# Performance work log

Measured on AMD Instinct MI355X. Metric: run time of the kernel, lower is better.

## Reference

```python
import jax, jax.numpy as jnp
import numpy as np

B, S, D, H, DFF, L = 16, 1024, 64, 4, 256, 2
DEPTH = D // H
C1, C2, NOUT = 64, 64, 1
EPS = 1e-6


def setup_inputs() -> dict:
    key = jax.random.key(0)
    ks = jax.random.split(key, 24)
    s = 0.02
    vals = jax.random.normal(ks[0], (B, S), jnp.float32)
    nanp = jax.random.uniform(ks[1], (B, S)) < 0.1
    inputs = jnp.where(nanp, jnp.nan, vals)
    inp = {
        'inputs': inputs,
        'embedding': jax.random.normal(ks[2], (S, D - 1), jnp.float32) * s,
        'wq': jax.random.normal(ks[3], (L, D, D), jnp.float32) * s,
        'wq_b': jnp.zeros((L, D), jnp.float32),
        'wk': jax.random.normal(ks[4], (L, D, D), jnp.float32) * s,
        'wk_b': jnp.zeros((L, D), jnp.float32),
        'wv': jax.random.normal(ks[5], (L, D, D), jnp.float32) * s,
        'wv_b': jnp.zeros((L, D), jnp.float32),
        'wo': jax.random.normal(ks[6], (L, D, D), jnp.float32) * s,
        'ffn_w1': jax.random.normal(ks[7], (L, D, DFF), jnp.float32) * s,
        'ffn_w2': jax.random.normal(ks[8], (L, DFF, D), jnp.float32) * s,
        'ln1_g': jnp.ones((L, D), jnp.float32),
        'ln1_b': jnp.zeros((L, D), jnp.float32),
        'ln2_g': jnp.ones((L, D), jnp.float32),
        'ln2_b': jnp.zeros((L, D), jnp.float32),
        'c_w1': jax.random.normal(ks[9], (D, C1), jnp.float32) * s,
        'c_b1': jnp.zeros((C1,), jnp.float32),
        'c_w2': jax.random.normal(ks[10], (C1, C2), jnp.float32) * s,
        'c_b2': jnp.zeros((C2,), jnp.float32),
        'c_w3': jax.random.normal(ks[11], (C2, NOUT), jnp.float32) * s,
        'c_b3': jnp.zeros((NOUT,), jnp.float32),
        'out_bias': jax.random.normal(ks[12], (1, NOUT), jnp.float32),
    }
    return inp


def _layer_norm(x, g, b):
    m = jnp.mean(x, axis=-1, keepdims=True)
    v = jnp.mean((x - m) ** 2, axis=-1, keepdims=True)
    return (x - m) / jnp.sqrt(v + EPS) * g + b


def _forward(inputs, embedding, wq, wq_b, wk, wk_b, wv, wv_b, wo,
             ffn_w1, ffn_w2, ln1_g, ln1_b, ln2_g, ln2_b,
             c_w1, c_b1, c_w2, c_b2, c_w3, c_b3, out_bias):
    nan_mask = jnp.isnan(inputs)                           # (B,S) bool
    x_in = jnp.where(nan_mask, jnp.zeros_like(inputs), inputs)
    # mask (B,1,S,S): masked if either attribute i or j is NaN
    mask = (nan_mask[:, :, None] | nan_mask[:, None, :]).astype(jnp.float32)[:, None, :, :]
    # keep factor: zeros out NaN attribute rows after each sub-block  (B,S,1)
    keep = 1.0 - jnp.transpose(jnp.prod(mask, axis=-1), (0, 2, 1))

    # positional/attribute embedding: table * sqrt(d-1) * sqrt(d)
    attr = embedding * jnp.sqrt(jnp.float32(D - 1)) * jnp.sqrt(jnp.float32(D))  # (S, D-1)
    attr = jnp.broadcast_to(attr[None], (B, S, D - 1))
    x = jnp.concatenate([attr, x_in[:, :, None]], axis=2)  # (B,S,D)
    x = x * keep

    scale = 1.0 / jnp.sqrt(jnp.float32(DEPTH))
    for i in range(L):
        q = (x @ wq[i] + wq_b[i]).reshape(B, S, H, DEPTH).transpose(0, 2, 1, 3)
        k = (x @ wk[i] + wk_b[i]).reshape(B, S, H, DEPTH).transpose(0, 2, 1, 3)
        v = (x @ wv[i] + wv_b[i]).reshape(B, S, H, DEPTH).transpose(0, 2, 1, 3)
        logits = jnp.einsum('bhqd,bhkd->bhqk', q, k) * scale + mask * (-1e9)
        attn = jax.nn.softmax(logits, axis=-1) * (1.0 - mask)  # post-softmax multiplicative mask
        ctx = jnp.einsum('bhqk,bhkd->bhqd', attn, v)
        ctx = ctx.transpose(0, 2, 1, 3).reshape(B, S, D) @ wo[i]
        out1 = _layer_norm(x + ctx, ln1_g[i], ln1_b[i]) * keep
        ffn = jax.nn.relu(out1 @ ffn_w1[i]) @ ffn_w2[i]
        x = _layer_norm(out1 + ffn, ln2_g[i], ln2_b[i]) * keep

    h = jax.nn.relu(x @ c_w1 + c_b1)
    h = jax.nn.relu(h @ c_w2 + c_b2)
    phi = h @ c_w3 + c_b3                                   # (B,S,NOUT)
    y = jnp.sum(phi, axis=1) + out_bias                     # (B,NOUT)
    return y


def reference(inputs, embedding, wq, wq_b, wk, wk_b, wv, wv_b, wo,
              ffn_w1, ffn_w2, ln1_g, ln1_b, ln2_g, ln2_b,
              c_w1, c_b1, c_w2, c_b2, c_w3, c_b3, out_bias):
    return _forward(inputs, embedding, wq, wq_b, wk, wk_b, wv, wv_b, wo,
                    ffn_w1, ffn_w2, ln1_g, ln1_b, ln2_g, ln2_b,
                    c_w1, c_b1, c_w2, c_b2, c_w3, c_b3, out_bias)
```

## Files before the change

### kernel.cpp

```cpp
#include <hip/hip_runtime.h>
#include <hip/hip_bf16.h>
#include <math.h>

#define BB 16
#define SS 1024
#define DD 64
#define HH 4
#define DEPTH 16
#define DFF 256
#define NROWS (BB*SS)
#define EPSV 1e-6f
#define NKSPLIT 8
#define KCHUNK (SS / NKSPLIT)

__device__ __forceinline__ float bcast(float x, int kk) {
  return __int_as_float(__builtin_amdgcn_readlane(__float_as_int(x), kk));
}

__global__ __launch_bounds__(256) void build_x_kernel(
    const float* __restrict__ inputs, const float* __restrict__ emb,
    float* __restrict__ x, float* __restrict__ keep) {
  int gid = blockIdx.x * 256 + threadIdx.x;
  int row = gid >> 6;
  int d = gid & 63;
  int s = row & (SS - 1);
  float vin = inputs[row];
  bool nan = __builtin_isnan(vin);
  float kp = nan ? 0.0f : 1.0f;
  if (d == 0) keep[row] = kp;
  float val;
  if (d < 63) {
    const float scale = 7.93725393319377f * 8.0f;
    val = emb[s * 63 + d] * scale;
  } else {
    val = nan ? 0.0f : vin;
  }
  x[row * 64 + d] = val * kp;
}

__global__ __launch_bounds__(64, 2) void qkv_kernel(
    const float* __restrict__ xin,
    const float* __restrict__ wq, const float* __restrict__ wqb,
    const float* __restrict__ wk, const float* __restrict__ wkb,
    const float* __restrict__ wv, const float* __restrict__ wvb,
    float* __restrict__ q, float* __restrict__ k, float* __restrict__ v) {
  int lane = threadIdx.x;
  float wqc[64], wkc[64], wvc[64];
#pragma unroll
  for (int kk = 0; kk < 64; ++kk) {
    wqc[kk] = wq[kk * 64 + lane];
    wkc[kk] = wk[kk * 64 + lane];
    wvc[kk] = wv[kk * 64 + lane];
  }
  float bq = wqb[lane], bk = wkb[lane], bv = wvb[lane];
  int h = lane >> 4, dep = lane & 15;
  int row0 = blockIdx.x * 8;
  for (int r = row0; r < row0 + 8; ++r) {
    float xr = xin[r * 64 + lane];
    float qa0 = 0.f, qa1 = 0.f, ka0 = 0.f, ka1 = 0.f, va0 = 0.f, va1 = 0.f;
#pragma unroll
    for (int kk = 0; kk < 64; kk += 2) {
      float x0 = bcast(xr, kk);
      float x1 = bcast(xr, kk + 1);
      qa0 = fmaf(x0, wqc[kk], qa0); qa1 = fmaf(x1, wqc[kk + 1], qa1);
      ka0 = fmaf(x0, wkc[kk], ka0); ka1 = fmaf(x1, wkc[kk + 1], ka1);
      va0 = fmaf(x0, wvc[kk], va0); va1 = fmaf(x1, wvc[kk + 1], va1);
    }
    int b = r >> 10, s = r & (SS - 1);
    size_t o = (size_t)(((b * HH + h) * SS + s)) * DEPTH + dep;
    q[o] = qa0 + qa1 + bq;
    k[o] = ka0 + ka1 + bk;
    v[o] = va0 + va1 + bv;
  }
}

__global__ __launch_bounds__(256) void attn_partial_kernel(
    const float* __restrict__ q, const float* __restrict__ k,
    const float* __restrict__ v, const float* __restrict__ keep,
    float* __restrict__ pA, float* __restrict__ pL) {
  __shared__ float klds[KCHUNK * DEPTH];
  __shared__ float vlds[KCHUNK * DEPTH];
  __shared__ float kplds[KCHUNK];
  int tid = threadIdx.x;
  int p = blockIdx.x * 256 + tid;
  int c = blockIdx.y;
  int bh = p >> 9;
  int s0 = p & 511;
  int b = bh >> 2;

  const float4* kbase = (const float4*)(k + ((size_t)bh * SS + c * KCHUNK) * DEPTH);
  const float4* vbase = (const float4*)(v + ((size_t)bh * SS + c * KCHUNK) * DEPTH);
#pragma unroll
  for (int i = 0; i < KCHUNK * 4 / 256; ++i) {
    ((float4*)klds)[tid + i * 256] = kbase[tid + i * 256];
    ((float4*)vlds)[tid + i * 256] = vbase[tid + i * 256];
  }
  if (tid < KCHUNK) kplds[tid] = keep[b * SS + c * KCHUNK + tid];
  __syncthreads();

  size_t rowA = (size_t)bh * SS + s0;
  size_t rowB = rowA + 512;
  const float4* qa4 = (const float4*)(q + rowA * DEPTH);
  const float4* qb4 = (const float4*)(q + rowB * DEPTH);
  float4 qA0 = qa4[0], qA1 = qa4[1], qA2 = qa4[2], qA3 = qa4[3];
  float4 qB0 = qb4[0], qB1 = qb4[1], qB2 = qb4[2], qB3 = qb4[3];
  float4 z = make_float4(0.f, 0.f, 0.f, 0.f);
  float4 aA0 = z, aA1 = z, aA2 = z, aA3 = z;
  float4 aB0 = z, aB1 = z, aB2 = z, aB3 = z;
  float lA = 0.0f, lB = 0.0f;
  for (int j = 0; j < KCHUNK; ++j) {
    const float4* kl = (const float4*)&klds[j * DEPTH];
    float4 k0 = kl[0], k1 = kl[1], k2 = kl[2], k3 = kl[3];
    const float4* vl = (const float4*)&vlds[j * DEPTH];
    float4 v0 = vl[0], v1 = vl[1], v2 = vl[2], v3 = vl[3];
    float dA0 = qA0.x * k0.x, dA1 = qA2.x * k2.x;
    float dB0 = qB0.x * k0.x, dB1 = qB2.x * k2.x;
    dA0 = fmaf(qA0.y, k0.y, dA0); dA1 = fmaf(qA2.y, k2.y, dA1);
    dB0 = fmaf(qB0.y, k0.y, dB0); dB1 = fmaf(qB2.y, k2.y, dB1);
    dA0 = fmaf(qA0.z, k0.z, dA0); dA1 = fmaf(qA2.z, k2.z, dA1);
    dB0 = fmaf(qB0.z, k0.z, dB0); dB1 = fmaf(qB2.z, k2.z, dB1);
    dA0 = fmaf(qA0.w, k0.w, dA0); dA1 = fmaf(qA2.w, k2.w, dA1);
    dB0 = fmaf(qB0.w, k0.w, dB0); dB1 = fmaf(qB2.w, k2.w, dB1);
    dA0 = fmaf(qA1.x, k1.x, dA0); dA1 = fmaf(qA3.x, k3.x, dA1);
    dB0 = fmaf(qB1.x, k1.x, dB0); dB1 = fmaf(qB3.x, k3.x, dB1);
    dA0 = fmaf(qA1.y, k1.y, dA0); dA1 = fmaf(qA3.y, k3.y, dA1);
    dB0 = fmaf(qB1.y, k1.y, dB0); dB1 = fmaf(qB3.y, k3.y, dB1);
    dA0 = fmaf(qA1.z, k1.z, dA0); dA1 = fmaf(qA3.z, k3.z, dA1);
    dB0 = fmaf(qB1.z, k1.z, dB0); dB1 = fmaf(qB3.z, k3.z, dB1);
    dA0 = fmaf(qA1.w, k1.w, dA0); dA1 = fmaf(qA3.w, k3.w, dA1);
    dB0 = fmaf(qB1.w, k1.w, dB0); dB1 = fmaf(qB3.w, k3.w, dB1);
    float kpj = kplds[j];
    float pa = __expf((dA0 + dA1) * 0.25f) * kpj;
    float pb = __expf((dB0 + dB1) * 0.25f) * kpj;
    lA += pa; lB += pb;
    aA0.x = fmaf(pa, v0.x, aA0.x); aB0.x = fmaf(pb, v0.x, aB0.x);
    aA0.y = fmaf(pa, v0.y, aA0.y); aB0.y = fmaf(pb, v0.y, aB0.y);
    aA0.z = fmaf(pa, v0.z, aA0.z); aB0.z = fmaf(pb, v0.z, aB0.z);
    aA0.w = fmaf(pa, v0.w, aA0.w); aB0.w = fmaf(pb, v0.w, aB0.w);
    aA1.x = fmaf(pa, v1.x, aA1.x); aB1.x = fmaf(pb, v1.x, aB1.x);
    aA1.y = fmaf(pa, v1.y, aA1.y); aB1.y = fmaf(pb, v1.y, aB1.y);
    aA1.z = fmaf(pa, v1.z, aA1.z); aB1.z = fmaf(pb, v1.z, aB1.z);
    aA1.w = fmaf(pa, v1.w, aA1.w); aB1.w = fmaf(pb, v1.w, aB1.w);
    aA2.x = fmaf(pa, v2.x, aA2.x); aB2.x = fmaf(pb, v2.x, aB2.x);
    aA2.y = fmaf(pa, v2.y, aA2.y); aB2.y = fmaf(pb, v2.y, aB2.y);
    aA2.z = fmaf(pa, v2.z, aA2.z); aB2.z = fmaf(pb, v2.z, aB2.z);
    aA2.w = fmaf(pa, v2.w, aA2.w); aB2.w = fmaf(pb, v2.w, aB2.w);
    aA3.x = fmaf(pa, v3.x, aA3.x); aB3.x = fmaf(pb, v3.x, aB3.x);
    aA3.y = fmaf(pa, v3.y, aA3.y); aB3.y = fmaf(pb, v3.y, aB3.y);
    aA3.z = fmaf(pa, v3.z, aA3.z); aB3.z = fmaf(pb, v3.z, aB3.z);
    aA3.w = fmaf(pa, v3.w, aA3.w); aB3.w = fmaf(pb, v3.w, aB3.w);
  }
  size_t oA = ((size_t)c << 16) + rowA;
  size_t oB = ((size_t)c << 16) + rowB;
  pL[oA] = lA; pL[oB] = lB;
  float4* o4a = (float4*)(pA + oA * 16);
  o4a[0] = aA0; o4a[1] = aA1; o4a[2] = aA2; o4a[3] = aA3;
  float4* o4b = (float4*)(pA + oB * 16);
  o4b[0] = aB0; o4b[1] = aB1; o4b[2] = aB2; o4b[3] = aB3;
}

__global__ __launch_bounds__(256) void wo_ln1_kernel(
    const float* __restrict__ pA, const float* __restrict__ pL,
    const float* __restrict__ xin,
    const float* __restrict__ wo, const float* __restrict__ g,
    const float* __restrict__ bta, const float* __restrict__ keep,
    float* __restrict__ out1) {
  int tid = threadIdx.x;
  int lane = tid & 63;
  float woc[64];
#pragma unroll
  for (int kk = 0; kk < 64; ++kk) woc[kk] = wo[kk * 64 + lane];
  float gg = g[lane], bb = bta[lane];
  int wave = tid >> 6;
  int row0 = blockIdx.x * 16 + wave * 4;
  for (int r = row0; r < row0 + 4; ++r) {
    int b = r >> 10, s = r & (SS - 1);
    int h = lane >> 4, dep = lane & 15;
    size_t rowi = ((size_t)(b * HH + h) << 10) + s;
    float num = 0.0f, den = 0.0f;
#pragma unroll
    for (int c = 0; c < NKSPLIT; ++c) {
      num += pA[(((size_t)c << 16) + rowi) * 16 + dep];
      den += pL[((size_t)c << 16) + rowi];
    }
    float cr = num * keep[r] / den;
    float a0 = 0.f, a1 = 0.f;
#pragma unroll
    for (int kk = 0; kk < 64; kk += 2) {
      a0 = fmaf(bcast(cr, kk), woc[kk], a0);
      a1 = fmaf(bcast(cr, kk + 1), woc[kk + 1], a1);
    }
    float t = a0 + a1 + xin[r * 64 + lane];
    float sum = t;
#pragma unroll
    for (int off = 32; off; off >>= 1) sum += __shfl_xor(sum, off, 64);
    float mean = sum * (1.0f / 64.0f);
    float dv = t - mean;
    float sq = dv * dv;
#pragma unroll
    for (int off = 32; off; off >>= 1) sq += __shfl_xor(sq, off, 64);
    float var = sq * (1.0f / 64.0f);
    float o = dv * rsqrtf(var + EPSV) * gg + bb;
    out1[r * 64 + lane] = o * keep[r];
  }
}

__global__ __launch_bounds__(256) void ffn_fused_kernel(
    const float* __restrict__ out1, const float* __restrict__ w1,
    const float* __restrict__ w2, const float* __restrict__ g,
    const float* __restrict__ bta, const float* __restrict__ keep,
    float* __restrict__ xout) {
  __shared__ float part[4][4][64];
  int tid = threadIdx.x, wave = tid >> 6, lane = tid & 63;
  float w1c[64], w2c[64];
#pragma unroll
  for (int kk = 0; kk < 64; ++kk)
    w1c[kk] = w1[kk * 256 + wave * 64 + lane];
#pragma unroll
  for (int j = 0; j < 64; ++j)
    w2c[j] = w2[(wave * 64 + j) * 64 + lane];
  float gg = g[lane], bb = bta[lane];
  int row0 = blockIdx.x * 16;
  for (int grp = 0; grp < 4; ++grp) {
    int rbase = row0 + grp * 4;
    float xr0 = out1[(rbase + 0) * 64 + lane];
    float xr1 = out1[(rbase + 1) * 64 + lane];
    float xr2 = out1[(rbase + 2) * 64 + lane];
    float xr3 = out1[(rbase + 3) * 64 + lane];
    float xrs[4] = {xr0, xr1, xr2, xr3};
#pragma unroll
    for (int r = 0; r < 4; ++r) {
      float h0 = 0.f, h1 = 0.f;
#pragma unroll
      for (int kk = 0; kk < 64; kk += 2) {
        h0 = fmaf(bcast(xrs[r], kk), w1c[kk], h0);
        h1 = fmaf(bcast(xrs[r], kk + 1), w1c[kk + 1], h1);
      }
      float hv = fmaxf(h0 + h1, 0.0f);
      float y0 = 0.f, y1 = 0.f;
#pragma unroll
      for (int j = 0; j < 64; j += 2) {
        y0 = fmaf(bcast(hv, j), w2c[j], y0);
        y1 = fmaf(bcast(hv, j + 1), w2c[j + 1], y1);
      }
      part[r][wave][lane] = y0 + y1;
    }
    __syncthreads();
    float xres = (wave == 0) ? xr0 : (wave == 1) ? xr1 : (wave == 2) ? xr2 : xr3;
    float t = part[wave][0][lane] + part[wave][1][lane] +
              part[wave][2][lane] + part[wave][3][lane] + xres;
    float sum = t;
#pragma unroll
    for (int off = 32; off; off >>= 1) sum += __shfl_xor(sum, off, 64);
    float mean = sum * (1.0f / 64.0f);
    float dv = t - mean;
    float sq = dv * dv;
#pragma unroll
    for (int off = 32; off; off >>= 1) sq += __shfl_xor(sq, off, 64);
    float var = sq * (1.0f / 64.0f);
    float o = dv * rsqrtf(var + EPSV) * gg + bb;
    xout[(rbase + wave) * 64 + lane] = o * keep[rbase + wave];
    __syncthreads();
  }
}

__global__ void init_out_kernel(const float* __restrict__ out_bias,
                                float* __restrict__ out) {
  if (threadIdx.x < BB) out[threadIdx.x] = out_bias[0];
}

__global__ __launch_bounds__(256, 3) void classifier_kernel(
    const float* __restrict__ x,
    const float* __restrict__ w1, const float* __restrict__ b1,
    const float* __restrict__ w2, const float* __restrict__ b2,
    const float* __restrict__ w3, const float* __restrict__ b3,
    float* __restrict__ out) {
  int tid = threadIdx.x;
  int lane = tid & 63, wave = tid >> 6;
  float w1c[64], w2c[64];
#pragma unroll
  for (int kk = 0; kk < 64; ++kk) {
    w1c[kk] = w1[kk * 64 + lane];
    w2c[kk] = w2[kk * 64 + lane];
  }
  float w3d = w3[lane];
  float bb1 = b1[lane], bb2 = b2[lane], b3v = b3[0];
  int row0 = blockIdx.x * 32 + wave * 8;
  float wavesum = 0.0f;
  for (int r = row0; r < row0 + 8; ++r) {
    float xr = x[r * 64 + lane];
    float h1a = 0.f, h1b = 0.f;
#pragma unroll
    for (int kk = 0; kk < 64; kk += 2) {
      h1a = fmaf(bcast(xr, kk), w1c[kk], h1a);
      h1b = fmaf(bcast(xr, kk + 1), w1c[kk + 1], h1b);
    }
    float h1 = fmaxf(h1a + h1b + bb1, 0.0f);
    float h2a = 0.f, h2b = 0.f;
#pragma unroll
    for (int kk = 0; kk < 64; kk += 2) {
      h2a = fmaf(bcast(h1, kk), w2c[kk], h2a);
      h2b = fmaf(bcast(h1, kk + 1), w2c[kk + 1], h2b);
    }
    float h2 = fmaxf(h2a + h2b + bb2, 0.0f);
    float p = h2 * w3d;
#pragma unroll
    for (int off = 32; off; off >>= 1) p += __shfl_xor(p, off, 64);
    wavesum += p + b3v;
  }
  if (lane == 0) {
    int b = row0 >> 10;
    atomicAdd(&out[b], wavesum);
  }
}

extern "C" void kernel_launch(void* const* d_in, const int* in_sizes, int n_in,
                              void* d_out, int out_size, void* d_ws, size_t ws_size,
                              hipStream_t stream) {
  const float* inputs = (const float*)d_in[0];
  const float* emb    = (const float*)d_in[1];
  const float* wq     = (const float*)d_in[2];
  const float* wqb    = (const float*)d_in[3];
  const float* wk     = (const float*)d_in[4];
  const float* wkb    = (const float*)d_in[5];
  const float* wv     = (const float*)d_in[6];
  const float* wvb    = (const float*)d_in[7];
  const float* wo     = (const float*)d_in[8];
  const float* fw1    = (const float*)d_in[9];
  const float* fw2    = (const float*)d_in[10];
  const float* l1g    = (const float*)d_in[11];
  const float* l1b    = (const float*)d_in[12];
  const float* l2g    = (const float*)d_in[13];
  const float* l2b    = (const float*)d_in[14];
  const float* cw1    = (const float*)d_in[15];
  const float* cb1    = (const float*)d_in[16];
  const float* cw2    = (const float*)d_in[17];
  const float* cb2    = (const float*)d_in[18];
  const float* cw3    = (const float*)d_in[19];
  const float* cb3    = (const float*)d_in[20];
  const float* obias  = (const float*)d_in[21];
  float* out = (float*)d_out;

  float* ws   = (float*)d_ws;
  float* x    = ws;
  float* keep = x    + (size_t)NROWS * 64;
  float* q    = keep + NROWS;
  float* k    = q    + (size_t)NROWS * 64;
  float* v    = k    + (size_t)NROWS * 64;
  float* out1 = v    + (size_t)NROWS * 64;
  float* pA   = out1 + (size_t)NROWS * 64;
  float* pL   = pA   + (size_t)NKSPLIT * 65536 * 16;

  build_x_kernel<<<4096, 256, 0, stream>>>(inputs, emb, x, keep);

  for (int i = 0; i < 2; ++i) {
    qkv_kernel<<<2048, 64, 0, stream>>>(
        x, wq + i * 4096, wqb + i * 64, wk + i * 4096, wkb + i * 64,
        wv + i * 4096, wvb + i * 64, q, k, v);
    attn_partial_kernel<<<dim3(128, NKSPLIT), 256, 0, stream>>>(
        q, k, v, keep, pA, pL);
    wo_ln1_kernel<<<1024, 256, 0, stream>>>(
        pA, pL, x, wo + i * 4096, l1g + i * 64, l1b + i * 64, keep, out1);
    ffn_fused_kernel<<<1024, 256, 0, stream>>>(
        out1, fw1 + i * 16384, fw2 + i * 16384, l2g + i * 64, l2b + i * 64,
        keep, x);
  }

  init_out_kernel<<<1, 64, 0, stream>>>(obias, out);
  classifier_kernel<<<512, 256, 0, stream>>>(x, cw1, cb1, cw2, cb2, cw3, cb3, out);
}
```

Baseline: 424.4 us.

## Use one query per attention thread and uniform float4 row loads in matvecs

The attention partial kernel now handles one query row per thread instead of two. It doubles the grid and adds a launch bound of 8 blocks per CU to raise occupancy, at the cost of reloading K/V tiles into LDS twice as often. The qkv, FFN and classifier kernels drop the readlane broadcast of a per-lane row element. They instead load the whole input row as wave-uniform float4 reads, trading cross-lane broadcasts for redundant cached memory loads.

```diff
diff --git a/kernel.cpp b/kernel.cpp
--- a/kernel.cpp
+++ b/kernel.cpp
@@ -56,15 +56,17 @@
   int h = lane >> 4, dep = lane & 15;
   int row0 = blockIdx.x * 8;
   for (int r = row0; r < row0 + 8; ++r) {
-    float xr = xin[r * 64 + lane];
+    const float4* xu = (const float4*)&xin[r * 64];
     float qa0 = 0.f, qa1 = 0.f, ka0 = 0.f, ka1 = 0.f, va0 = 0.f, va1 = 0.f;
 #pragma unroll
-    for (int kk = 0; kk < 64; kk += 2) {
-      float x0 = bcast(xr, kk);
-      float x1 = bcast(xr, kk + 1);
-      qa0 = fmaf(x0, wqc[kk], qa0); qa1 = fmaf(x1, wqc[kk + 1], qa1);
-      ka0 = fmaf(x0, wkc[kk], ka0); ka1 = fmaf(x1, wkc[kk + 1], ka1);
-      va0 = fmaf(x0, wvc[kk], va0); va1 = fmaf(x1, wvc[kk + 1], va1);
+    for (int t = 0; t < 16; ++t) {
+      float4 xv = xu[t];
+      qa0 = fmaf(xv.x, wqc[4*t+0], qa0); qa1 = fmaf(xv.y, wqc[4*t+1], qa1);
+      qa0 = fmaf(xv.z, wqc[4*t+2], qa0); qa1 = fmaf(xv.w, wqc[4*t+3], qa1);
+      ka0 = fmaf(xv.x, wkc[4*t+0], ka0); ka1 = fmaf(xv.y, wkc[4*t+1], ka1);
+      ka0 = fmaf(xv.z, wkc[4*t+2], ka0); ka1 = fmaf(xv.w, wkc[4*t+3], ka1);
+      va0 = fmaf(xv.x, wvc[4*t+0], va0); va1 = fmaf(xv.y, wvc[4*t+1], va1);
+      va0 = fmaf(xv.z, wvc[4*t+2], va0); va1 = fmaf(xv.w, wvc[4*t+3], va1);
     }
     int b = r >> 10, s = r & (SS - 1);
     size_t o = (size_t)(((b * HH + h) * SS + s)) * DEPTH + dep;
@@ -74,7 +76,7 @@
   }
 }
 
-__global__ __launch_bounds__(256) void attn_partial_kernel(
+__global__ __launch_bounds__(256, 8) void attn_partial_kernel(
     const float* __restrict__ q, const float* __restrict__ k,
     const float* __restrict__ v, const float* __restrict__ keep,
     float* __restrict__ pA, float* __restrict__ pL) {
@@ -82,10 +84,9 @@
   __shared__ float vlds[KCHUNK * DEPTH];
   __shared__ float kplds[KCHUNK];
   int tid = threadIdx.x;
-  int p = blockIdx.x * 256 + tid;
+  int grow = blockIdx.x * 256 + tid;
   int c = blockIdx.y;
-  int bh = p >> 9;
-  int s0 = p & 511;
+  int bh = grow >> 10;
   int b = bh >> 2;
 
   const float4* kbase = (const float4*)(k + ((size_t)bh * SS + c * KCHUNK) * DEPTH);
@@ -98,65 +99,39 @@
   if (tid < KCHUNK) kplds[tid] = keep[b * SS + c * KCHUNK + tid];
   __syncthreads();
 
-  size_t rowA = (size_t)bh * SS + s0;
-  size_t rowB = rowA + 512;
-  const float4* qa4 = (const float4*)(q + rowA * DEPTH);
-  const float4* qb4 = (const float4*)(q + rowB * DEPTH);
-  float4 qA0 = qa4[0], qA1 = qa4[1], qA2 = qa4[2], qA3 = qa4[3];
-  float4 qB0 = qb4[0], qB1 = qb4[1], qB2 = qb4[2], qB3 = qb4[3];
+  const float4* q4 = (const float4*)(q + (size_t)grow * DEPTH);
+  float4 q0 = q4[0], q1 = q4[1], q2 = q4[2], q3 = q4[3];
   float4 z = make_float4(0.f, 0.f, 0.f, 0.f);
-  float4 aA0 = z, aA1 = z, aA2 = z, aA3 = z;
-  float4 aB0 = z, aB1 = z, aB2 = z, aB3 = z;
-  float lA = 0.0f, lB = 0.0f;
+  float4 a0 = z, a1 = z, a2 = z, a3 = z;
+  float l = 0.0f;
   for (int j = 0; j < KCHUNK; ++j) {
     const float4* kl = (const float4*)&klds[j * DEPTH];
     float4 k0 = kl[0], k1 = kl[1], k2 = kl[2], k3 = kl[3];
     const float4* vl = (const float4*)&vlds[j * DEPTH];
     float4 v0 = vl[0], v1 = vl[1], v2 = vl[2], v3 = vl[3];
-    float dA0 = qA0.x * k0.x, dA1 = qA2.x * k2.x;
-    float dB0 = qB0.x * k0.x, dB1 = qB2.x * k2.x;
-    dA0 = fmaf(qA0.y, k0.y, dA0); dA1 = fmaf(qA2.y, k2.y, dA1);
-    dB0 = fmaf(qB0.y, k0.y, dB0); dB1 = fmaf(qB2.y, k2.y, dB1);
-    dA0 = fmaf(qA0.z, k0.z, dA0); dA1 = fmaf(qA2.z, k2.z, dA1);
-    dB0 = fmaf(qB0.z, k0.z, dB0); dB1 = fmaf(qB2.z, k2.z, dB1);
-    dA0 = fmaf(qA0.w, k0.w, dA0); dA1 = fmaf(qA2.w, k2.w, dA1);
-    dB0 = fmaf(qB0.w, k0.w, dB0); dB1 = fmaf(qB2.w, k2.w, dB1);
-    dA0 = fmaf(qA1.x, k1.x, dA0); dA1 = fmaf(qA3.x, k3.x, dA1);
-    dB0 = fmaf(qB1.x, k1.x, dB0); dB1 = fmaf(qB3.x, k3.x, dB1);
-    dA0 = fmaf(qA1.y, k1.y, dA0); dA1 = fmaf(qA3.y, k3.y, dA1);
-    dB0 = fmaf(qB1.y, k1.y, dB0); dB1 = fmaf(qB3.y, k3.y, dB1);
-    dA0 = fmaf(qA1.z, k1.z, dA0); dA1 = fmaf(qA3.z, k3.z, dA1);
-    dB0 = fmaf(qB1.z, k1.z, dB0); dB1 = fmaf(qB3.z, k3.z, dB1);
-    dA0 = fmaf(qA1.w, k1.w, dA0); dA1 = fmaf(qA3.w, k3.w, dA1);
-    dB0 = fmaf(qB1.w, k1.w, dB0); dB1 = fmaf(qB3.w, k3.w, dB1);
-    float kpj = kplds[j];
-    float pa = __expf((dA0 + dA1) * 0.25f) * kpj;
-    float pb = __expf((dB0 + dB1) * 0.25f) * kpj;
-    lA += pa; lB += pb;
-    aA0.x = fmaf(pa, v0.x, aA0.x); aB0.x = fmaf(pb, v0.x, aB0.x);
-    aA0.y = fmaf(pa, v0.y, aA0.y); aB0.y = fmaf(pb, v0.y, aB0.y);
-    aA0.z = fmaf(pa, v0.z, aA0.z); aB0.z = fmaf(pb, v0.z, aB0.z);
-    aA0.w = fmaf(pa, v0.w, aA0.w); aB0.w = fmaf(pb, v0.w, aB0.w);
-    aA1.x = fmaf(pa, v1.x, aA1.x); aB1.x = fmaf(pb, v1.x, aB1.x);
-    aA1.y = fmaf(pa, v1.y, aA1.y); aB1.y = fmaf(pb, v1.y, aB1.y);
-    aA1.z = fmaf(pa, v1.z, aA1.z); aB1.z = fmaf(pb, v1.z, aB1.z);
-    aA1.w = fmaf(pa, v1.w, aA1.w); aB1.w = fmaf(pb, v1.w, aB1.w);
-    aA2.x = fmaf(pa, v2.x, aA2.x); aB2.x = fmaf(pb, v2.x, aB2.x);
-    aA2.y = fmaf(pa, v2.y, aA2.y); aB2.y = fmaf(pb, v2.y, aB2.y);
-    aA2.z = fmaf(pa, v2.z, aA2.z); aB2.z = fmaf(pb, v2.z, aB2.z);
-    aA2.w = fmaf(pa, v2.w, aA2.w); aB2.w = fmaf(pb, v2.w, aB2.w);
-    aA3.x = fmaf(pa, v3.x, aA3.x); aB3.x = fmaf(pb, v3.x, aB3.x);
-    aA3.y = fmaf(pa, v3.y, aA3.y); aB3.y = fmaf(pb, v3.y, aB3.y);
-    aA3.z = fmaf(pa, v3.z, aA3.z); aB3.z = fmaf(pb, v3.z, aB3.z);
-    aA3.w = fmaf(pa, v3.w, aA3.w); aB3.w = fmaf(pb, v3.w, aB3.w);
-  }
-  size_t oA = ((size_t)c << 16) + rowA;
-  size_t oB = ((size_t)c << 16) + rowB;
-  pL[oA] = lA; pL[oB] = lB;
-  float4* o4a = (float4*)(pA + oA * 16);
-  o4a[0] = aA0; o4a[1] = aA1; o4a[2] = aA2; o4a[3] = aA3;
-  float4* o4b = (float4*)(pA + oB * 16);
-  o4b[0] = aB0; o4b[1] = aB1; o4b[2] = aB2; o4b[3] = aB3;
+    float d0 = q0.x * k0.x, d1 = q2.x * k2.x;
+    d0 = fmaf(q0.y, k0.y, d0); d1 = fmaf(q2.y, k2.y, d1);
+    d0 = fmaf(q0.z, k0.z, d0); d1 = fmaf(q2.z, k2.z, d1);
+    d0 = fmaf(q0.w, k0.w, d0); d1 = fmaf(q2.w, k2.w, d1);
+    d0 = fmaf(q1.x, k1.x, d0); d1 = fmaf(q3.x, k3.x, d1);
+    d0 = fmaf(q1.y, k1.y, d0); d1 = fmaf(q3.y, k3.y, d1);
+    d0 = fmaf(q1.z, k1.z, d0); d1 = fmaf(q3.z, k3.z, d1);
+    d0 = fmaf(q1.w, k1.w, d0); d1 = fmaf(q3.w, k3.w, d1);
+    float p = __expf((d0 + d1) * 0.25f) * kplds[j];
+    l += p;
+    a0.x = fmaf(p, v0.x, a0.x); a0.y = fmaf(p, v0.y, a0.y);
+    a0.z = fmaf(p, v0.z, a0.z); a0.w = fmaf(p, v0.w, a0.w);
+    a1.x = fmaf(p, v1.x, a1.x); a1.y = fmaf(p, v1.y, a1.y);
+    a1.z = fmaf(p, v1.z, a1.z); a1.w = fmaf(p, v1.w, a1.w);
+    a2.x = fmaf(p, v2.x, a2.x); a2.y = fmaf(p, v2.y, a2.y);
+    a2.z = fmaf(p, v2.z, a2.z); a2.w = fmaf(p, v2.w, a2.w);
+    a3.x = fmaf(p, v3.x, a3.x); a3.y = fmaf(p, v3.y, a3.y);
+    a3.z = fmaf(p, v3.z, a3.z); a3.w = fmaf(p, v3.w, a3.w);
+  }
+  size_t orow = ((size_t)c << 16) + grow;
+  pL[orow] = l;
+  float4* o4 = (float4*)(pA + orow * 16);
+  o4[0] = a0; o4[1] = a1; o4[2] = a2; o4[3] = a3;
 }
 
 __global__ __launch_bounds__(256) void wo_ln1_kernel(
@@ -223,18 +198,15 @@
   int row0 = blockIdx.x * 16;
   for (int grp = 0; grp < 4; ++grp) {
     int rbase = row0 + grp * 4;
-    float xr0 = out1[(rbase + 0) * 64 + lane];
-    float xr1 = out1[(rbase + 1) * 64 + lane];
-    float xr2 = out1[(rbase + 2) * 64 + lane];
-    float xr3 = out1[(rbase + 3) * 64 + lane];
-    float xrs[4] = {xr0, xr1, xr2, xr3};
 #pragma unroll
     for (int r = 0; r < 4; ++r) {
+      const float4* xu = (const float4*)&out1[(rbase + r) * 64];
       float h0 = 0.f, h1 = 0.f;
 #pragma unroll
-      for (int kk = 0; kk < 64; kk += 2) {
-        h0 = fmaf(bcast(xrs[r], kk), w1c[kk], h0);
-        h1 = fmaf(bcast(xrs[r], kk + 1), w1c[kk + 1], h1);
+      for (int t = 0; t < 16; ++t) {
+        float4 xv = xu[t];
+        h0 = fmaf(xv.x, w1c[4*t+0], h0); h1 = fmaf(xv.y, w1c[4*t+1], h1);
+        h0 = fmaf(xv.z, w1c[4*t+2], h0); h1 = fmaf(xv.w, w1c[4*t+3], h1);
       }
       float hv = fmaxf(h0 + h1, 0.0f);
       float y0 = 0.f, y1 = 0.f;
@@ -246,7 +218,7 @@
       part[r][wave][lane] = y0 + y1;
     }
     __syncthreads();
-    float xres = (wave == 0) ? xr0 : (wave == 1) ? xr1 : (wave == 2) ? xr2 : xr3;
+    float xres = out1[(rbase + wave) * 64 + lane];
     float t = part[wave][0][lane] + part[wave][1][lane] +
               part[wave][2][lane] + part[wave][3][lane] + xres;
     float sum = t;
@@ -288,12 +260,13 @@
   int row0 = blockIdx.x * 32 + wave * 8;
   float wavesum = 0.0f;
   for (int r = row0; r < row0 + 8; ++r) {
-    float xr = x[r * 64 + lane];
+    const float4* xu = (const float4*)&x[r * 64];
     float h1a = 0.f, h1b = 0.f;
 #pragma unroll
-    for (int kk = 0; kk < 64; kk += 2) {
-      h1a = fmaf(bcast(xr, kk), w1c[kk], h1a);
-      h1b = fmaf(bcast(xr, kk + 1), w1c[kk + 1], h1b);
+    for (int t = 0; t < 16; ++t) {
+      float4 xv = xu[t];
+      h1a = fmaf(xv.x, w1c[4*t+0], h1a); h1b = fmaf(xv.y, w1c[4*t+1], h1b);
+      h1a = fmaf(xv.z, w1c[4*t+2], h1a); h1b = fmaf(xv.w, w1c[4*t+3], h1b);
     }
     float h1 = fmaxf(h1a + h1b + bb1, 0.0f);
     float h2a = 0.f, h2b = 0.f;
@@ -357,7 +330,7 @@
     qkv_kernel<<<2048, 64, 0, stream>>>(
         x, wq + i * 4096, wqb + i * 64, wk + i * 4096, wkb + i * 64,
         wv + i * 4096, wvb + i * 64, q, k, v);
-    attn_partial_kernel<<<dim3(128, NKSPLIT), 256, 0, stream>>>(
+    attn_partial_kernel<<<dim3(256, NKSPLIT), 256, 0, stream>>>(
         q, k, v, keep, pA, pL);
     wo_ln1_kernel<<<1024, 256, 0, stream>>>(
         pA, pL, x, wo + i * 4096, l1g + i * 64, l1b + i * 64, keep, out1);
```

After: 627.5 us. +47.8%, slower.

## Split QKV projection across waves with LDS row staging; LDS broadcast in Wo

Applied to the files above, without the earlier changes.

The QKV kernel now gives each of three waves one of the Q/K/V weight matrices and stages 16 input rows in shared memory, so each wave holds 64 weight registers instead of 192. Row values are read as float4 from LDS instead of readlane broadcasts, and the Wo+LN1 kernel uses the same LDS broadcast for its context vector. Attention dot products are collapsed into a single accumulator chain, and occupancy hints are added to the launch bounds. The aim is less register pressure, higher occupancy and fewer scalar readlane instructions, at the cost of longer dependency chains in attention and extra LDS traffic.

```diff
diff --git a/kernel.cpp b/kernel.cpp
--- a/kernel.cpp
+++ b/kernel.cpp
@@ -38,48 +38,51 @@
   x[row * 64 + d] = val * kp;
 }
 
-__global__ __launch_bounds__(64, 2) void qkv_kernel(
+__global__ __launch_bounds__(192, 4) void qkv_kernel(
     const float* __restrict__ xin,
     const float* __restrict__ wq, const float* __restrict__ wqb,
     const float* __restrict__ wk, const float* __restrict__ wkb,
     const float* __restrict__ wv, const float* __restrict__ wvb,
     float* __restrict__ q, float* __restrict__ k, float* __restrict__ v) {
-  int lane = threadIdx.x;
-  float wqc[64], wkc[64], wvc[64];
-#pragma unroll
-  for (int kk = 0; kk < 64; ++kk) {
-    wqc[kk] = wq[kk * 64 + lane];
-    wkc[kk] = wk[kk * 64 + lane];
-    wvc[kk] = wv[kk * 64 + lane];
-  }
-  float bq = wqb[lane], bk = wkb[lane], bv = wvb[lane];
+  __shared__ __align__(16) float xlds[16 * 64];
+  int tid = threadIdx.x;
+  int wave = tid >> 6, lane = tid & 63;
+  const float* wsel = (wave == 0) ? wq : (wave == 1) ? wk : wv;
+  const float* bsel = (wave == 0) ? wqb : (wave == 1) ? wkb : wvb;
+  float* outp = (wave == 0) ? q : (wave == 1) ? k : v;
+  float wc[64];
+#pragma unroll
+  for (int kk = 0; kk < 64; ++kk) wc[kk] = wsel[kk * 64 + lane];
+  float bias = bsel[lane];
+  int row0 = blockIdx.x * 16;
+  for (int i = tid; i < 256; i += 192)
+    ((float4*)xlds)[i] = ((const float4*)(xin + (size_t)row0 * 64))[i];
+  __syncthreads();
   int h = lane >> 4, dep = lane & 15;
-  int row0 = blockIdx.x * 8;
-  for (int r = row0; r < row0 + 8; ++r) {
-    float xr = xin[r * 64 + lane];
-    float qa0 = 0.f, qa1 = 0.f, ka0 = 0.f, ka1 = 0.f, va0 = 0.f, va1 = 0.f;
-#pragma unroll
-    for (int kk = 0; kk < 64; kk += 2) {
-      float x0 = bcast(xr, kk);
-      float x1 = bcast(xr, kk + 1);
-      qa0 = fmaf(x0, wqc[kk], qa0); qa1 = fmaf(x1, wqc[kk + 1], qa1);
-      ka0 = fmaf(x0, wkc[kk], ka0); ka1 = fmaf(x1, wkc[kk + 1], ka1);
-      va0 = fmaf(x0, wvc[kk], va0); va1 = fmaf(x1, wvc[kk + 1], va1);
+  for (int rr = 0; rr < 16; ++rr) {
+    int r = row0 + rr;
+    const float4* xu = (const float4*)&xlds[rr * 64];
+    float a0 = 0.f, a1 = 0.f, a2 = 0.f, a3 = 0.f;
+#pragma unroll
+    for (int t = 0; t < 16; ++t) {
+      float4 xv = xu[t];
+      a0 = fmaf(xv.x, wc[4 * t + 0], a0);
+      a1 = fmaf(xv.y, wc[4 * t + 1], a1);
+      a2 = fmaf(xv.z, wc[4 * t + 2], a2);
+      a3 = fmaf(xv.w, wc[4 * t + 3], a3);
     }
     int b = r >> 10, s = r & (SS - 1);
     size_t o = (size_t)(((b * HH + h) * SS + s)) * DEPTH + dep;
-    q[o] = qa0 + qa1 + bq;
-    k[o] = ka0 + ka1 + bk;
-    v[o] = va0 + va1 + bv;
-  }
-}
-
-__global__ __launch_bounds__(256) void attn_partial_kernel(
+    outp[o] = (a0 + a1) + (a2 + a3) + bias;
+  }
+}
+
+__global__ __launch_bounds__(256, 4) void attn_partial_kernel(
     const float* __restrict__ q, const float* __restrict__ k,
     const float* __restrict__ v, const float* __restrict__ keep,
     float* __restrict__ pA, float* __restrict__ pL) {
-  __shared__ float klds[KCHUNK * DEPTH];
-  __shared__ float vlds[KCHUNK * DEPTH];
+  __shared__ __align__(16) float klds[KCHUNK * DEPTH];
+  __shared__ __align__(16) float vlds[KCHUNK * DEPTH];
   __shared__ float kplds[KCHUNK];
   int tid = threadIdx.x;
   int p = blockIdx.x * 256 + tid;
@@ -113,25 +116,25 @@
     float4 k0 = kl[0], k1 = kl[1], k2 = kl[2], k3 = kl[3];
     const float4* vl = (const float4*)&vlds[j * DEPTH];
     float4 v0 = vl[0], v1 = vl[1], v2 = vl[2], v3 = vl[3];
-    float dA0 = qA0.x * k0.x, dA1 = qA2.x * k2.x;
-    float dB0 = qB0.x * k0.x, dB1 = qB2.x * k2.x;
-    dA0 = fmaf(qA0.y, k0.y, dA0); dA1 = fmaf(qA2.y, k2.y, dA1);
-    dB0 = fmaf(qB0.y, k0.y, dB0); dB1 = fmaf(qB2.y, k2.y, dB1);
-    dA0 = fmaf(qA0.z, k0.z, dA0); dA1 = fmaf(qA2.z, k2.z, dA1);
-    dB0 = fmaf(qB0.z, k0.z, dB0); dB1 = fmaf(qB2.z, k2.z, dB1);
-    dA0 = fmaf(qA0.w, k0.w, dA0); dA1 = fmaf(qA2.w, k2.w, dA1);
-    dB0 = fmaf(qB0.w, k0.w, dB0); dB1 = fmaf(qB2.w, k2.w, dB1);
-    dA0 = fmaf(qA1.x, k1.x, dA0); dA1 = fmaf(qA3.x, k3.x, dA1);
-    dB0 = fmaf(qB1.x, k1.x, dB0); dB1 = fmaf(qB3.x, k3.x, dB1);
-    dA0 = fmaf(qA1.y, k1.y, dA0); dA1 = fmaf(qA3.y, k3.y, dA1);
-    dB0 = fmaf(qB1.y, k1.y, dB0); dB1 = fmaf(qB3.y, k3.y, dB1);
-    dA0 = fmaf(qA1.z, k1.z, dA0); dA1 = fmaf(qA3.z, k3.z, dA1);
-    dB0 = fmaf(qB1.z, k1.z, dB0); dB1 = fmaf(qB3.z, k3.z, dB1);
-    dA0 = fmaf(qA1.w, k1.w, dA0); dA1 = fmaf(qA3.w, k3.w, dA1);
-    dB0 = fmaf(qB1.w, k1.w, dB0); dB1 = fmaf(qB3.w, k3.w, dB1);
+    float dA = qA0.x * k0.x, dB = qB0.x * k0.x;
+    dA = fmaf(qA0.y, k0.y, dA); dB = fmaf(qB0.y, k0.y, dB);
+    dA = fmaf(qA0.z, k0.z, dA); dB = fmaf(qB0.z, k0.z, dB);
+    dA = fmaf(qA0.w, k0.w, dA); dB = fmaf(qB0.w, k0.w, dB);
+    dA = fmaf(qA1.x, k1.x, dA); dB = fmaf(qB1.x, k1.x, dB);
+    dA = fmaf(qA1.y, k1.y, dA); dB = fmaf(qB1.y, k1.y, dB);
+    dA = fmaf(qA1.z, k1.z, dA); dB = fmaf(qB1.z, k1.z, dB);
+    dA = fmaf(qA1.w, k1.w, dA); dB = fmaf(qB1.w, k1.w, dB);
+    dA = fmaf(qA2.x, k2.x, dA); dB = fmaf(qB2.x, k2.x, dB);
+    dA = fmaf(qA2.y, k2.y, dA); dB = fmaf(qB2.y, k2.y, dB);
+    dA = fmaf(qA2.z, k2.z, dA); dB = fmaf(qB2.z, k2.z, dB);
+    dA = fmaf(qA2.w, k2.w, dA); dB = fmaf(qB2.w, k2.w, dB);
+    dA = fmaf(qA3.x, k3.x, dA); dB = fmaf(qB3.x, k3.x, dB);
+    dA = fmaf(qA3.y, k3.y, dA); dB = fmaf(qB3.y, k3.y, dB);
+    dA = fmaf(qA3.z, k3.z, dA); dB = fmaf(qB3.z, k3.z, dB);
+    dA = fmaf(qA3.w, k3.w, dA); dB = fmaf(qB3.w, k3.w, dB);
     float kpj = kplds[j];
-    float pa = __expf((dA0 + dA1) * 0.25f) * kpj;
-    float pb = __expf((dB0 + dB1) * 0.25f) * kpj;
+    float pa = __expf(dA * 0.25f) * kpj;
+    float pb = __expf(dB * 0.25f) * kpj;
     lA += pa; lB += pb;
     aA0.x = fmaf(pa, v0.x, aA0.x); aB0.x = fmaf(pb, v0.x, aB0.x);
     aA0.y = fmaf(pa, v0.y, aA0.y); aB0.y = fmaf(pb, v0.y, aB0.y);
@@ -159,23 +162,24 @@
   o4b[0] = aB0; o4b[1] = aB1; o4b[2] = aB2; o4b[3] = aB3;
 }
 
-__global__ __launch_bounds__(256) void wo_ln1_kernel(
+__global__ __launch_bounds__(256, 4) void wo_ln1_kernel(
     const float* __restrict__ pA, const float* __restrict__ pL,
     const float* __restrict__ xin,
     const float* __restrict__ wo, const float* __restrict__ g,
     const float* __restrict__ bta, const float* __restrict__ keep,
     float* __restrict__ out1) {
+  __shared__ __align__(16) float ctxlds[4][64];
   int tid = threadIdx.x;
-  int lane = tid & 63;
+  int wave = tid >> 6, lane = tid & 63;
   float woc[64];
 #pragma unroll
   for (int kk = 0; kk < 64; ++kk) woc[kk] = wo[kk * 64 + lane];
   float gg = g[lane], bb = bta[lane];
-  int wave = tid >> 6;
+  int h = lane >> 4, dep = lane & 15;
   int row0 = blockIdx.x * 16 + wave * 4;
-  for (int r = row0; r < row0 + 4; ++r) {
+  for (int rr = 0; rr < 4; ++rr) {
+    int r = row0 + rr;
     int b = r >> 10, s = r & (SS - 1);
-    int h = lane >> 4, dep = lane & 15;
     size_t rowi = ((size_t)(b * HH + h) << 10) + s;
     float num = 0.0f, den = 0.0f;
 #pragma unroll
@@ -184,18 +188,23 @@
       den += pL[((size_t)c << 16) + rowi];
     }
     float cr = num * keep[r] / den;
-    float a0 = 0.f, a1 = 0.f;
-#pragma unroll
-    for (int kk = 0; kk < 64; kk += 2) {
-      a0 = fmaf(bcast(cr, kk), woc[kk], a0);
-      a1 = fmaf(bcast(cr, kk + 1), woc[kk + 1], a1);
-    }
-    float t = a0 + a1 + xin[r * 64 + lane];
-    float sum = t;
+    ctxlds[wave][lane] = cr;
+    const float4* cu = (const float4*)ctxlds[wave];
+    float a0 = 0.f, a1 = 0.f, a2 = 0.f, a3 = 0.f;
+#pragma unroll
+    for (int t = 0; t < 16; ++t) {
+      float4 cv = cu[t];
+      a0 = fmaf(cv.x, woc[4 * t + 0], a0);
+      a1 = fmaf(cv.y, woc[4 * t + 1], a1);
+      a2 = fmaf(cv.z, woc[4 * t + 2], a2);
+      a3 = fmaf(cv.w, woc[4 * t + 3], a3);
+    }
+    float t_ = (a0 + a1) + (a2 + a3) + xin[r * 64 + lane];
+    float sum = t_;
 #pragma unroll
     for (int off = 32; off; off >>= 1) sum += __shfl_xor(sum, off, 64);
     float mean = sum * (1.0f / 64.0f);
-    float dv = t - mean;
+    float dv = t_ - mean;
     float sq = dv * dv;
 #pragma unroll
     for (int off = 32; off; off >>= 1) sq += __shfl_xor(sq, off, 64);
@@ -354,7 +363,7 @@
   build_x_kernel<<<4096, 256, 0, stream>>>(inputs, emb, x, keep);
 
   for (int i = 0; i < 2; ++i) {
-    qkv_kernel<<<2048, 64, 0, stream>>>(
+    qkv_kernel<<<1024, 192, 0, stream>>>(
         x, wq + i * 4096, wqb + i * 64, wk + i * 4096, wkb + i * 64,
         wv + i * 4096, wvb + i * 64, q, k, v);
     attn_partial_kernel<<<dim3(128, NKSPLIT), 256, 0, stream>>>(
```

Result: slower. 503.2 us (+18.6%).
